# Kernel tuning notes

Measured on AMD Instinct MI355X. Metric: run time of the kernel, lower is better.

Reference implementation:

```python
import jax, jax.numpy as jnp
import numpy as np

N_NODES = 50000
N_EDGES = 1600000
IN_DIM, HIDDEN, OUT_DIM = 128, 128, 64


def setup_inputs() -> dict:
    key = jax.random.key(0)
    ks = jax.random.split(key, 8)
    x = jax.random.normal(ks[0], (N_NODES, IN_DIM), dtype=jnp.float32)
    edge_index = jax.random.randint(ks[1], (2, N_EDGES), 0, N_NODES, dtype=jnp.int64)
    # SAGEConv params: lin_l applied to aggregated neighbors (with bias),
    # lin_r applied to root/self features (no bias) -- PyG defaults.
    def lin_init(k, fan_in, fan_out):
        bound = 1.0 / np.sqrt(fan_in)
        return jax.random.uniform(k, (fan_in, fan_out), jnp.float32, -bound, bound)
    W1_l = lin_init(ks[2], IN_DIM, HIDDEN)
    W1_r = lin_init(ks[3], IN_DIM, HIDDEN)
    b1 = jnp.zeros((HIDDEN,), jnp.float32)
    W2_l = lin_init(ks[4], HIDDEN, OUT_DIM)
    W2_r = lin_init(ks[5], HIDDEN, OUT_DIM)
    b2 = jnp.zeros((OUT_DIM,), jnp.float32)
    return {"x": x, "edge_index": edge_index, "W1_l": W1_l, "W1_r": W1_r,
            "b1": b1, "W2_l": W2_l, "W2_r": W2_r, "b2": b2}


def _sage_conv(h, src, dst, n_nodes, W_l, W_r, b):
    # gather messages from source nodes, mean-aggregate at destinations
    msg = h[src]                                              # [E, D]
    agg_sum = jax.ops.segment_sum(msg, dst, num_segments=n_nodes)
    deg = jax.ops.segment_sum(jnp.ones((src.shape[0],), h.dtype), dst,
                              num_segments=n_nodes)
    agg_mean = agg_sum / jnp.maximum(deg, 1.0)[:, None]       # [N, D]
    return agg_mean @ W_l + h @ W_r + b


def reference(x, edge_index, W1_l, W1_r, b1, W2_l, W2_r, b2):
    n = x.shape[0]
    src, dst = edge_index[0], edge_index[1]
    h = jax.nn.relu(_sage_conv(x, src, dst, n, W1_l, W1_r, b1))
    return _sage_conv(h, src, dst, n, W2_l, W2_r, b2)
```

## Files before the change

### kernel.cpp

```cpp
#include <hip/hip_runtime.h>

#define NN 50000
#define NE 1600000
#define BSTRIDE 96
#define C_BKT 196
#define P1_BLKS 512
#define P1_CHUNK 3125
#define CAP 56
#define XCVT_BLKS 1563
#define WCVT_BLKS 48
#define PP_PREP (XCVT_BLKS + WCVT_BLKS)

typedef __bf16 bf16x8 __attribute__((ext_vector_type(8)));
typedef float  f32x4  __attribute__((ext_vector_type(4)));
typedef float  f32x2  __attribute__((ext_vector_type(2)));

__device__ __forceinline__ float bfLo(uint u) { union { uint i; float f; } v; v.i = u << 16; return v.f; }
__device__ __forceinline__ float bfHi(uint u) { union { uint i; float f; } v; v.i = u & 0xffff0000u; return v.f; }
__device__ __forceinline__ float bf1(ushort s) { union { uint i; float f; } v; v.i = (uint)s << 16; return v.f; }
__device__ __forceinline__ ushort f2bf(float f) {
    union { float f; uint i; } v; v.f = f;
    uint r = v.i + 0x7fffu + ((v.i >> 16) & 1u);
    return (ushort)(r >> 16);
}
__device__ __forceinline__ uint pack2(float a, float b) {
    return (uint)f2bf(a) | ((uint)f2bf(b) << 16);
}
__device__ __forceinline__ bf16x8 load8(const ushort* p) {
    union { uint4 u; bf16x8 b; } v; v.u = *(const uint4*)p; return v.b;
}

#define ACC8(u) { a0 += bfLo(u.x); a1 += bfHi(u.x); a2 += bfLo(u.y); a3 += bfHi(u.y); \
                  a4 += bfLo(u.z); a5 += bfHi(u.z); a6 += bfLo(u.w); a7 += bfHi(u.w); }

#define CVA(u, o) { f32x2 p0 = __builtin_amdgcn_cvt_pk_f32_fp8((int)(u), 0); \
                    f32x2 p1 = __builtin_amdgcn_cvt_pk_f32_fp8((int)(u), 1); \
                    a[(o)+0] += p0.x; a[(o)+1] += p0.y; a[(o)+2] += p1.x; a[(o)+3] += p1.y; }
#define ACCF8(v) { CVA((v).x, 0); CVA((v).y, 4); CVA((v).z, 8); CVA((v).w, 12); }

__global__ __launch_bounds__(1024) void k_pp(
    const float4* __restrict__ x, ushort4* __restrict__ xb, uint* __restrict__ xf8,
    const float* __restrict__ W1l, const float* __restrict__ W1r,
    const float* __restrict__ W2l, const float* __restrict__ W2r,
    ushort* __restrict__ T1l, ushort* __restrict__ T1r,
    ushort* __restrict__ T2l, ushort* __restrict__ T2r,
    const int* __restrict__ src, const int* __restrict__ dst,
    uint* __restrict__ cells, ushort* __restrict__ cnt) {
    __shared__ uint hist[C_BKT];
    const int b = blockIdx.x;
    const int tid = threadIdx.x;
    if (b < XCVT_BLKS) {
        int i = b * 1024 + tid;
        if (i < NN * 128 / 4) {
            float4 v = x[i];
            ushort4 o; o.x = f2bf(v.x); o.y = f2bf(v.y); o.z = f2bf(v.z); o.w = f2bf(v.w);
            xb[i] = o;
            uint r = (uint)__builtin_amdgcn_cvt_pk_fp8_f32(v.x, v.y, 0, 0);
            r = (uint)__builtin_amdgcn_cvt_pk_fp8_f32(v.z, v.w, (int)r, 1);
            xf8[i] = r;
        }
    } else if (b < PP_PREP) {
        int i = (b - XCVT_BLKS) * 1024 + tid;
        if (i < 16384) {
            int k = i >> 7, n = i & 127; T1l[n * 128 + k] = f2bf(W1l[i]);
        } else if (i < 32768) {
            int j = i - 16384; int k = j >> 7, n = j & 127; T1r[n * 128 + k] = f2bf(W1r[j]);
        } else if (i < 40960) {
            int j = i - 32768; int k = j >> 6, n = j & 63;  T2l[n * 128 + k] = f2bf(W2l[j]);
        } else {
            int j = i - 40960; int k = j >> 6, n = j & 63;  T2r[n * 128 + k] = f2bf(W2r[j]);
        }
    } else {
        const int b2 = b - PP_PREP;
        for (int i = tid; i < C_BKT; i += 1024) hist[i] = 0;
        __syncthreads();
        const int beg = b2 * P1_CHUNK;
        uint* myCells = cells + (size_t)b2 * C_BKT * CAP;
        for (int i = beg + tid; i < beg + P1_CHUNK; i += 1024) {
            int d = dst[i];
            int s = src[i];
            int c = d >> 8;
            uint p = atomicAdd(&hist[c], 1);
            if (p < CAP) myCells[c * CAP + p] = ((uint)(d & 255) << 16) | (uint)s;
        }
        __syncthreads();
        for (int i = tid; i < C_BKT; i += 1024)
            cnt[(size_t)b2 * C_BKT + i] = (ushort)min(hist[i], (uint)CAP);
    }
}

__global__ __launch_bounds__(1024) void k_part2(const uint* __restrict__ cells,
                        const ushort* __restrict__ cnt,
                        ushort* __restrict__ col, int* __restrict__ deg) {
    __shared__ uint hist[256];
    const int c = blockIdx.x;
    if (threadIdx.x < 256) hist[threadIdx.x] = 0;
    __syncthreads();
    const int b = threadIdx.x >> 1;
    const int sub = threadIdx.x & 1;
    const uint* cell = cells + ((size_t)b * C_BKT + c) * CAP;
    const int n = cnt[(size_t)b * C_BKT + c];
    const int nodeBase = c << 8;
    for (int j = sub; j < n; j += 2) {
        uint e = cell[j];
        int dl = e >> 16;
        uint p = atomicAdd(&hist[dl], 1);
        if (p < BSTRIDE)
            col[(size_t)(nodeBase + dl) * BSTRIDE + p] = (ushort)(e & 0xFFFF);
    }
    __syncthreads();
    if (threadIdx.x < 256) {
        int node = nodeBase + threadIdx.x;
        if (node < NN) deg[node] = (int)hist[threadIdx.x];
    }
}

__global__ void k_agg128(const uchar* __restrict__ xf8, const ushort* __restrict__ col,
                         const int* __restrict__ deg, ushort* __restrict__ out) {
    int node = (blockIdx.x * blockDim.x + threadIdx.x) >> 6;
    int lane = threadIdx.x & 63;
    int q = lane >> 3;
    int c = lane & 7;
    int d = deg[node];
    int dd = min(d, BSTRIDE);
    const ushort* cb = col + (size_t)node * BSTRIDE;
    float a[16];
    #pragma unroll
    for (int i = 0; i < 16; i++) a[i] = 0.f;
    for (int j0 = 0; j0 < dd; j0 += 64) {
        int idx = (j0 + lane < dd) ? (int)cb[j0 + lane] : 0;
        int cnt = min(64, dd - j0);
        int t = 0;
        for (; t + 16 <= cnt; t += 16) {
            int s0 = __shfl(idx, t + q);
            int s1 = __shfl(idx, t + 8 + q);
            uint4 u0 = *(const uint4*)(xf8 + (size_t)s0 * 128 + c * 16);
            uint4 u1 = *(const uint4*)(xf8 + (size_t)s1 * 128 + c * 16);
            ACCF8(u0); ACCF8(u1);
        }
        for (; t < cnt; t += 8) {
            int s = __shfl(idx, t + q);
            if (t + q < cnt) {
                uint4 u = *(const uint4*)(xf8 + (size_t)s * 128 + c * 16);
                ACCF8(u);
            }
        }
    }
    #pragma unroll
    for (int m = 8; m < 64; m <<= 1) {
        #pragma unroll
        for (int i = 0; i < 16; i++) a[i] += __shfl_xor(a[i], m);
    }
    if (q == 0) {
        float inv = 1.f / fmaxf((float)d, 1.f);
        uint4 o;
        o.x = pack2(a[0] * inv, a[1] * inv);
        o.y = pack2(a[2] * inv, a[3] * inv);
        o.z = pack2(a[4] * inv, a[5] * inv);
        o.w = pack2(a[6] * inv, a[7] * inv);
        *(uint4*)(out + (size_t)node * 128 + c * 16) = o;
        o.x = pack2(a[8] * inv, a[9] * inv);
        o.y = pack2(a[10] * inv, a[11] * inv);
        o.z = pack2(a[12] * inv, a[13] * inv);
        o.w = pack2(a[14] * inv, a[15] * inv);
        *(uint4*)(out + (size_t)node * 128 + c * 16 + 8) = o;
    }
}

#define PAD1 136
__global__ __launch_bounds__(256) void k_gemm12(
    const ushort* __restrict__ agg, const ushort* __restrict__ xb,
    const ushort* __restrict__ T1l, const ushort* __restrict__ T1r,
    const ushort* __restrict__ T2l, const ushort* __restrict__ T2r,
    const float* __restrict__ b1, const float* __restrict__ b2,
    ushort* __restrict__ hW, float* __restrict__ outp) {
    __shared__ ushort hS[2][16 * PAD1];
    const int lane = threadIdx.x & 63;
    const int wave = threadIdx.x >> 6;
    const int s = wave >> 1;
    const int ch = wave & 1;
    const int quad = lane >> 4, r16 = lane & 15;
    const int row0 = blockIdx.x * 32 + s * 16;
    const int arow = min(row0 + r16, NN - 1);
    ushort* myS = &hS[s][0];

    bf16x8 aAgg[4], aXb[4];
    #pragma unroll
    for (int kt = 0; kt < 4; kt++) {
        const int k = kt * 32 + quad * 8;
        aAgg[kt] = load8(agg + (size_t)arow * 128 + k);
        aXb[kt]  = load8(xb  + (size_t)arow * 128 + k);
    }

    f32x4 acc[4];
    #pragma unroll
    for (int nt = 0; nt < 4; nt++) acc[nt] = (f32x4){0.f, 0.f, 0.f, 0.f};
    #pragma unroll
    for (int kt = 0; kt < 4; kt++) {
        const int k = kt * 32 + quad * 8;
        #pragma unroll
        for (int nt = 0; nt < 4; nt++) {
            const int wr = ch * 64 + nt * 16 + r16;
            acc[nt] = __builtin_amdgcn_mfma_f32_16x16x32_bf16(aAgg[kt], load8(T1l + wr * 128 + k), acc[nt], 0, 0, 0);
            acc[nt] = __builtin_amdgcn_mfma_f32_16x16x32_bf16(aXb[kt],  load8(T1r + wr * 128 + k), acc[nt], 0, 0, 0);
        }
    }
    #pragma unroll
    for (int nt = 0; nt < 4; nt++) {
        int cc = ch * 64 + nt * 16 + r16;
        float bv = b1[cc];
        #pragma unroll
        for (int i = 0; i < 4; i++) {
            int lr = quad * 4 + i;
            myS[lr * PAD1 + cc] = f2bf(fmaxf(acc[nt][i] + bv, 0.f));
        }
    }
    __syncthreads();

    bf16x8 ah[4];
    #pragma unroll
    for (int kt = 0; kt < 4; kt++)
        ah[kt] = load8(&myS[r16 * PAD1 + kt * 32 + quad * 8]);

    f32x4 acc2[2], acc3[2];
    #pragma unroll
    for (int nt = 0; nt < 2; nt++) {
        acc2[nt] = (f32x4){0.f, 0.f, 0.f, 0.f};
        acc3[nt] = (f32x4){0.f, 0.f, 0.f, 0.f};
    }
    #pragma unroll
    for (int kt = 0; kt < 4; kt++) {
        const int k = kt * 32 + quad * 8;
        #pragma unroll
        for (int nt = 0; nt < 2; nt++) {
            const int wr = ch * 32 + nt * 16 + r16;
            acc2[nt] = __builtin_amdgcn_mfma_f32_16x16x32_bf16(ah[kt], load8(T2l + wr * 128 + k), acc2[nt], 0, 0, 0);
            acc3[nt] = __builtin_amdgcn_mfma_f32_16x16x32_bf16(ah[kt], load8(T2r + wr * 128 + k), acc3[nt], 0, 0, 0);
        }
    }
    #pragma unroll
    for (int nt = 0; nt < 2; nt++) {
        int cc = ch * 32 + nt * 16 + r16;
        float bv = b2[cc];
        #pragma unroll
        for (int i = 0; i < 4; i++) {
            int rr = row0 + quad * 4 + i;
            if (rr < NN) {
                hW[(size_t)rr * 64 + cc] = f2bf(acc2[nt][i]);
                outp[(size_t)rr * 64 + cc] = acc3[nt][i] + bv;
            }
        }
    }
}

__global__ void k_agg64f(const ushort* __restrict__ hW, const ushort* __restrict__ col,
                         const int* __restrict__ deg, const float* __restrict__ outp,
                         float* __restrict__ out) {
    int node = (blockIdx.x * blockDim.x + threadIdx.x) >> 6;
    int lane = threadIdx.x & 63;
    int q = lane >> 3;
    int c = lane & 7;
    int d = deg[node];
    int dd = min(d, BSTRIDE);
    const ushort* cb = col + (size_t)node * BSTRIDE;
    float a0=0.f,a1=0.f,a2=0.f,a3=0.f,a4=0.f,a5=0.f,a6=0.f,a7=0.f;
    for (int j0 = 0; j0 < dd; j0 += 64) {
        int idx = (j0 + lane < dd) ? (int)cb[j0 + lane] : 0;
        int cnt = min(64, dd - j0);
        int t = 0;
        for (; t + 16 <= cnt; t += 16) {
            int s0 = __shfl(idx, t + q);
            int s1 = __shfl(idx, t + 8 + q);
            uint4 u0 = *(const uint4*)(hW + (size_t)s0 * 64 + c * 8);
            uint4 u1 = *(const uint4*)(hW + (size_t)s1 * 64 + c * 8);
            ACC8(u0); ACC8(u1);
        }
        for (; t < cnt; t += 8) {
            int s = __shfl(idx, t + q);
            if (t + q < cnt) {
                uint4 u = *(const uint4*)(hW + (size_t)s * 64 + c * 8);
                ACC8(u);
            }
        }
    }
    #pragma unroll
    for (int m = 8; m < 64; m <<= 1) {
        a0 += __shfl_xor(a0, m); a1 += __shfl_xor(a1, m);
        a2 += __shfl_xor(a2, m); a3 += __shfl_xor(a3, m);
        a4 += __shfl_xor(a4, m); a5 += __shfl_xor(a5, m);
        a6 += __shfl_xor(a6, m); a7 += __shfl_xor(a7, m);
    }
    if (q == 0) {
        float inv = 1.f / fmaxf((float)d, 1.f);
        float4 p0 = *(const float4*)(outp + (size_t)node * 64 + c * 8);
        float4 p1 = *(const float4*)(outp + (size_t)node * 64 + c * 8 + 4);
        float4 o;
        o.x = a0 * inv + p0.x; o.y = a1 * inv + p0.y;
        o.z = a2 * inv + p0.z; o.w = a3 * inv + p0.w;
        *(float4*)(out + (size_t)node * 64 + c * 8) = o;
        o.x = a4 * inv + p1.x; o.y = a5 * inv + p1.y;
        o.z = a6 * inv + p1.z; o.w = a7 * inv + p1.w;
        *(float4*)(out + (size_t)node * 64 + c * 8 + 4) = o;
    }
}

extern "C" void kernel_launch(void* const* d_in, const int* in_sizes, int n_in,
                              void* d_out, int out_size, void* d_ws, size_t ws_size,
                              hipStream_t stream) {
    const float* x   = (const float*)d_in[0];
    const int*   ei  = (const int*)d_in[1];
    const float* W1l = (const float*)d_in[2];
    const float* W1r = (const float*)d_in[3];
    const float* b1  = (const float*)d_in[4];
    const float* W2l = (const float*)d_in[5];
    const float* W2r = (const float*)d_in[6];
    const float* b2  = (const float*)d_in[7];
    float* out = (float*)d_out;

    const int* src = ei;
    const int* dst = ei + NE;

    char* w = (char*)d_ws;
    ushort* col   = (ushort*)w;                  w += (size_t)NN * BSTRIDE * 2;
    int* deg      = (int*)w;                     w += (size_t)50048 * 4;
    ushort* cnt   = (ushort*)w;                  w += (size_t)P1_BLKS * C_BKT * 2;
    ushort* xb    = (ushort*)w;                  w += (size_t)NN * 128 * 2;
    ushort* T1l   = (ushort*)w;                  w += 128 * 128 * 2;
    ushort* T1r   = (ushort*)w;                  w += 128 * 128 * 2;
    ushort* T2l   = (ushort*)w;                  w += 64 * 128 * 2;
    ushort* T2r   = (ushort*)w;                  w += 64 * 128 * 2;
    ushort* agg1  = (ushort*)w;                  w += (size_t)NN * 128 * 2;
    ushort* hW    = (ushort*)w;                  w += (size_t)NN * 64 * 2;
    float* outp   = (float*)w;                   w += (size_t)NN * 64 * 4;
    uchar* xf8    = (uchar*)w;                   w += (size_t)NN * 128;
    uint* cells  = (uint*)agg1;

    k_pp<<<PP_PREP + P1_BLKS, 1024, 0, stream>>>(
        (const float4*)x, (ushort4*)xb, (uint*)xf8, W1l, W1r, W2l, W2r,
        T1l, T1r, T2l, T2r, src, dst, cells, cnt);
    k_part2<<<C_BKT, 1024, 0, stream>>>(cells, cnt, col, deg);

    k_agg128<<<NN / 4, 256, 0, stream>>>(xf8, col, deg, agg1);
    k_gemm12<<<(NN + 31) / 32, 256, 0, stream>>>(agg1, xb, T1l, T1r, T2l, T2r, b1, b2, hW, outp);

    k_agg64f<<<NN / 4, 256, 0, stream>>>(hW, col, deg, outp, out);
}
```

Before: 221.8 us.

## Store layer-2 messages as FP8 and root term as bf16, prefetch GEMM weights

The layer-2 projected features hW are now written as FP8 (e4m3) instead of bf16, and the root/bias partial outp as bf16 instead of fp32. This halves the gathered bytes in the second aggregation kernel, which now has each lane read 16 FP8 values and uses a 16-lane-per-edge layout. The GEMM kernel also preloads all weight fragments into registers before the MFMA loops and declares launch_bounds(256,1). This trades output accuracy for bandwidth, and higher register pressure may lower occupancy.

After: 236.1 us. 6.4% more time.

```diff
diff --git a/kernel.cpp b/kernel.cpp
--- a/kernel.cpp
+++ b/kernel.cpp
@@ -29,9 +29,9 @@
 __device__ __forceinline__ bf16x8 load8(const ushort* p) {
     union { uint4 u; bf16x8 b; } v; v.u = *(const uint4*)p; return v.b;
 }
-
-#define ACC8(u) { a0 += bfLo(u.x); a1 += bfHi(u.x); a2 += bfLo(u.y); a3 += bfHi(u.y); \
-                  a4 += bfLo(u.z); a5 += bfHi(u.z); a6 += bfLo(u.w); a7 += bfHi(u.w); }
+__device__ __forceinline__ uchar f2fp8(float v) {
+    return (uchar)((uint)__builtin_amdgcn_cvt_pk_fp8_f32(v, v, 0, 0) & 0xffu);
+}
 
 #define CVA(u, o) { f32x2 p0 = __builtin_amdgcn_cvt_pk_f32_fp8((int)(u), 0); \
                     f32x2 p1 = __builtin_amdgcn_cvt_pk_f32_fp8((int)(u), 1); \
@@ -168,12 +168,12 @@
 }
 
 #define PAD1 136
-__global__ __launch_bounds__(256) void k_gemm12(
+__global__ __launch_bounds__(256, 1) void k_gemm12(
     const ushort* __restrict__ agg, const ushort* __restrict__ xb,
     const ushort* __restrict__ T1l, const ushort* __restrict__ T1r,
     const ushort* __restrict__ T2l, const ushort* __restrict__ T2r,
     const float* __restrict__ b1, const float* __restrict__ b2,
-    ushort* __restrict__ hW, float* __restrict__ outp) {
+    uchar* __restrict__ hW8, ushort* __restrict__ outp) {
     __shared__ ushort hS[2][16 * PAD1];
     const int lane = threadIdx.x & 63;
     const int wave = threadIdx.x >> 6;
@@ -184,44 +184,51 @@
     const int arow = min(row0 + r16, NN - 1);
     ushort* myS = &hS[s][0];
 
-    bf16x8 aAgg[4], aXb[4];
+    bf16x8 aAgg[4], aXb[4], bl[4][4], br[4][4];
     #pragma unroll
     for (int kt = 0; kt < 4; kt++) {
         const int k = kt * 32 + quad * 8;
         aAgg[kt] = load8(agg + (size_t)arow * 128 + k);
         aXb[kt]  = load8(xb  + (size_t)arow * 128 + k);
-    }
-
-    f32x4 acc[4];
-    #pragma unroll
-    for (int nt = 0; nt < 4; nt++) acc[nt] = (f32x4){0.f, 0.f, 0.f, 0.f};
-    #pragma unroll
-    for (int kt = 0; kt < 4; kt++) {
-        const int k = kt * 32 + quad * 8;
         #pragma unroll
         for (int nt = 0; nt < 4; nt++) {
             const int wr = ch * 64 + nt * 16 + r16;
-            acc[nt] = __builtin_amdgcn_mfma_f32_16x16x32_bf16(aAgg[kt], load8(T1l + wr * 128 + k), acc[nt], 0, 0, 0);
-            acc[nt] = __builtin_amdgcn_mfma_f32_16x16x32_bf16(aXb[kt],  load8(T1r + wr * 128 + k), acc[nt], 0, 0, 0);
-        }
-    }
+            bl[kt][nt] = load8(T1l + wr * 128 + k);
+            br[kt][nt] = load8(T1r + wr * 128 + k);
+        }
+    }
+    f32x4 acc[4];
+    #pragma unroll
+    for (int nt = 0; nt < 4; nt++) acc[nt] = (f32x4){0.f, 0.f, 0.f, 0.f};
+    #pragma unroll
+    for (int kt = 0; kt < 4; kt++)
+        #pragma unroll
+        for (int nt = 0; nt < 4; nt++) {
+            acc[nt] = __builtin_amdgcn_mfma_f32_16x16x32_bf16(aAgg[kt], bl[kt][nt], acc[nt], 0, 0, 0);
+            acc[nt] = __builtin_amdgcn_mfma_f32_16x16x32_bf16(aXb[kt],  br[kt][nt], acc[nt], 0, 0, 0);
+        }
     #pragma unroll
     for (int nt = 0; nt < 4; nt++) {
         int cc = ch * 64 + nt * 16 + r16;
         float bv = b1[cc];
         #pragma unroll
-        for (int i = 0; i < 4; i++) {
-            int lr = quad * 4 + i;
-            myS[lr * PAD1 + cc] = f2bf(fmaxf(acc[nt][i] + bv, 0.f));
-        }
+        for (int i = 0; i < 4; i++)
+            myS[(quad * 4 + i) * PAD1 + cc] = f2bf(fmaxf(acc[nt][i] + bv, 0.f));
     }
     __syncthreads();
 
-    bf16x8 ah[4];
-    #pragma unroll
-    for (int kt = 0; kt < 4; kt++)
-        ah[kt] = load8(&myS[r16 * PAD1 + kt * 32 + quad * 8]);
-
+    bf16x8 ah[4], c2l[4][2], c2r[4][2];
+    #pragma unroll
+    for (int kt = 0; kt < 4; kt++) {
+        const int k = kt * 32 + quad * 8;
+        ah[kt] = load8(&myS[r16 * PAD1 + k]);
+        #pragma unroll
+        for (int nt = 0; nt < 2; nt++) {
+            const int wr = ch * 32 + nt * 16 + r16;
+            c2l[kt][nt] = load8(T2l + wr * 128 + k);
+            c2r[kt][nt] = load8(T2r + wr * 128 + k);
+        }
+    }
     f32x4 acc2[2], acc3[2];
     #pragma unroll
     for (int nt = 0; nt < 2; nt++) {
@@ -229,15 +236,12 @@
         acc3[nt] = (f32x4){0.f, 0.f, 0.f, 0.f};
     }
     #pragma unroll
-    for (int kt = 0; kt < 4; kt++) {
-        const int k = kt * 32 + quad * 8;
+    for (int kt = 0; kt < 4; kt++)
         #pragma unroll
         for (int nt = 0; nt < 2; nt++) {
-            const int wr = ch * 32 + nt * 16 + r16;
-            acc2[nt] = __builtin_amdgcn_mfma_f32_16x16x32_bf16(ah[kt], load8(T2l + wr * 128 + k), acc2[nt], 0, 0, 0);
-            acc3[nt] = __builtin_amdgcn_mfma_f32_16x16x32_bf16(ah[kt], load8(T2r + wr * 128 + k), acc3[nt], 0, 0, 0);
-        }
-    }
+            acc2[nt] = __builtin_amdgcn_mfma_f32_16x16x32_bf16(ah[kt], c2l[kt][nt], acc2[nt], 0, 0, 0);
+            acc3[nt] = __builtin_amdgcn_mfma_f32_16x16x32_bf16(ah[kt], c2r[kt][nt], acc3[nt], 0, 0, 0);
+        }
     #pragma unroll
     for (int nt = 0; nt < 2; nt++) {
         int cc = ch * 32 + nt * 16 + r16;
@@ -246,61 +250,67 @@
         for (int i = 0; i < 4; i++) {
             int rr = row0 + quad * 4 + i;
             if (rr < NN) {
-                hW[(size_t)rr * 64 + cc] = f2bf(acc2[nt][i]);
-                outp[(size_t)rr * 64 + cc] = acc3[nt][i] + bv;
+                hW8[(size_t)rr * 64 + cc] = f2fp8(acc2[nt][i]);
+                outp[(size_t)rr * 64 + cc] = f2bf(acc3[nt][i] + bv);
             }
         }
     }
 }
 
-__global__ void k_agg64f(const ushort* __restrict__ hW, const ushort* __restrict__ col,
-                         const int* __restrict__ deg, const float* __restrict__ outp,
+__global__ void k_agg64f(const uchar* __restrict__ hW8, const ushort* __restrict__ col,
+                         const int* __restrict__ deg, const ushort* __restrict__ outp,
                          float* __restrict__ out) {
     int node = (blockIdx.x * blockDim.x + threadIdx.x) >> 6;
     int lane = threadIdx.x & 63;
-    int q = lane >> 3;
-    int c = lane & 7;
+    int q = lane >> 2;
+    int c = lane & 3;
     int d = deg[node];
     int dd = min(d, BSTRIDE);
     const ushort* cb = col + (size_t)node * BSTRIDE;
-    float a0=0.f,a1=0.f,a2=0.f,a3=0.f,a4=0.f,a5=0.f,a6=0.f,a7=0.f;
+    float a[16];
+    #pragma unroll
+    for (int i = 0; i < 16; i++) a[i] = 0.f;
     for (int j0 = 0; j0 < dd; j0 += 64) {
         int idx = (j0 + lane < dd) ? (int)cb[j0 + lane] : 0;
         int cnt = min(64, dd - j0);
         int t = 0;
-        for (; t + 16 <= cnt; t += 16) {
+        for (; t + 32 <= cnt; t += 32) {
             int s0 = __shfl(idx, t + q);
-            int s1 = __shfl(idx, t + 8 + q);
-            uint4 u0 = *(const uint4*)(hW + (size_t)s0 * 64 + c * 8);
-            uint4 u1 = *(const uint4*)(hW + (size_t)s1 * 64 + c * 8);
-            ACC8(u0); ACC8(u1);
-        }
-        for (; t < cnt; t += 8) {
+            int s1 = __shfl(idx, t + 16 + q);
+            uint4 u0 = *(const uint4*)(hW8 + (size_t)s0 * 64 + c * 16);
+            uint4 u1 = *(const uint4*)(hW8 + (size_t)s1 * 64 + c * 16);
+            ACCF8(u0); ACCF8(u1);
+        }
+        for (; t < cnt; t += 16) {
             int s = __shfl(idx, t + q);
             if (t + q < cnt) {
-                uint4 u = *(const uint4*)(hW + (size_t)s * 64 + c * 8);
-                ACC8(u);
+                uint4 u = *(const uint4*)(hW8 + (size_t)s * 64 + c * 16);
+                ACCF8(u);
             }
         }
     }
     #pragma unroll
-    for (int m = 8; m < 64; m <<= 1) {
-        a0 += __shfl_xor(a0, m); a1 += __shfl_xor(a1, m);
-        a2 += __shfl_xor(a2, m); a3 += __shfl_xor(a3, m);
-        a4 += __shfl_xor(a4, m); a5 += __shfl_xor(a5, m);
-        a6 += __shfl_xor(a6, m); a7 += __shfl_xor(a7, m);
+    for (int m = 4; m < 64; m <<= 1) {
+        #pragma unroll
+        for (int i = 0; i < 16; i++) a[i] += __shfl_xor(a[i], m);
     }
     if (q == 0) {
         float inv = 1.f / fmaxf((float)d, 1.f);
-        float4 p0 = *(const float4*)(outp + (size_t)node * 64 + c * 8);
-        float4 p1 = *(const float4*)(outp + (size_t)node * 64 + c * 8 + 4);
+        uint4 p0 = *(const uint4*)(outp + (size_t)node * 64 + c * 16);
+        uint4 p1 = *(const uint4*)(outp + (size_t)node * 64 + c * 16 + 8);
         float4 o;
-        o.x = a0 * inv + p0.x; o.y = a1 * inv + p0.y;
-        o.z = a2 * inv + p0.z; o.w = a3 * inv + p0.w;
-        *(float4*)(out + (size_t)node * 64 + c * 8) = o;
-        o.x = a4 * inv + p1.x; o.y = a5 * inv + p1.y;
-        o.z = a6 * inv + p1.z; o.w = a7 * inv + p1.w;
-        *(float4*)(out + (size_t)node * 64 + c * 8 + 4) = o;
+        o.x = a[0] * inv + bfLo(p0.x); o.y = a[1] * inv + bfHi(p0.x);
+        o.z = a[2] * inv + bfLo(p0.y); o.w = a[3] * inv + bfHi(p0.y);
+        *(float4*)(out + (size_t)node * 64 + c * 16) = o;
+        o.x = a[4] * inv + bfLo(p0.z); o.y = a[5] * inv + bfHi(p0.z);
+        o.z = a[6] * inv + bfLo(p0.w); o.w = a[7] * inv + bfHi(p0.w);
+        *(float4*)(out + (size_t)node * 64 + c * 16 + 4) = o;
+        o.x = a[8] * inv + bfLo(p1.x); o.y = a[9] * inv + bfHi(p1.x);
+        o.z = a[10] * inv + bfLo(p1.y); o.w = a[11] * inv + bfHi(p1.y);
+        *(float4*)(out + (size_t)node * 64 + c * 16 + 8) = o;
+        o.x = a[12] * inv + bfLo(p1.z); o.y = a[13] * inv + bfHi(p1.z);
+        o.z = a[14] * inv + bfLo(p1.w); o.w = a[15] * inv + bfHi(p1.w);
+        *(float4*)(out + (size_t)node * 64 + c * 16 + 12) = o;
     }
 }
 
@@ -330,8 +340,9 @@
     ushort* T2l   = (ushort*)w;                  w += 64 * 128 * 2;
     ushort* T2r   = (ushort*)w;                  w += 64 * 128 * 2;
     ushort* agg1  = (ushort*)w;                  w += (size_t)NN * 128 * 2;
-    ushort* hW    = (ushort*)w;                  w += (size_t)NN * 64 * 2;
-    float* outp   = (float*)w;                   w += (size_t)NN * 64 * 4;
+    uchar* hW8    = (uchar*)w;                   w += (size_t)NN * 64;
+    ushort* outp  = (ushort*)w;                  w += (size_t)NN * 64 * 2;
+    w += 131072;
     uchar* xf8    = (uchar*)w;                   w += (size_t)NN * 128;
     uint* cells  = (uint*)agg1;
 
@@ -341,7 +352,7 @@
     k_part2<<<C_BKT, 1024, 0, stream>>>(cells, cnt, col, deg);
 
     k_agg128<<<NN / 4, 256, 0, stream>>>(xf8, col, deg, agg1);
-    k_gemm12<<<(NN + 31) / 32, 256, 0, stream>>>(agg1, xb, T1l, T1r, T2l, T2r, b1, b2, hW, outp);
-
-    k_agg64f<<<NN / 4, 256, 0, stream>>>(hW, col, deg, outp, out);
-}
+    k_gemm12<<<(NN + 31) / 32, 256, 0, stream>>>(agg1, xb, T1l, T1r, T2l, T2r, b1, b2, hW8, outp);
+
+    k_agg64f<<<NN / 4, 256, 0, stream>>>(hW8, col, deg, outp, out);
+}
```

## Store GEMM operands in MFMA-fragment-packed layout for contiguous per-lane loads

Applied to the files above, without the earlier changes.

The bf16 copy of x, the aggregated features and the transposed weights are now written in a tile-packed layout, where each 16-row by 32-k MFMA fragment is one contiguous 512-element block. Each lane then loads its 8 bf16 values at lane*8, so a wave reads 1 KB contiguously instead of strided row segments. The producer kernels (prep and agg128) take on the layout transform in their scattered writes, and the workspace grows slightly because rows are padded to a multiple of 16.

Result: faster. 198.0 us (-10.7%).

```diff
diff --git a/kernel.cpp b/kernel.cpp
--- a/kernel.cpp
+++ b/kernel.cpp
@@ -10,6 +10,7 @@
 #define XCVT_BLKS 1563
 #define WCVT_BLKS 48
 #define PP_PREP (XCVT_BLKS + WCVT_BLKS)
+#define RGRP 3128
 
 typedef __bf16 bf16x8 __attribute__((ext_vector_type(8)));
 typedef float  f32x4  __attribute__((ext_vector_type(4)));
@@ -17,7 +18,6 @@
 
 __device__ __forceinline__ float bfLo(uint u) { union { uint i; float f; } v; v.i = u << 16; return v.f; }
 __device__ __forceinline__ float bfHi(uint u) { union { uint i; float f; } v; v.i = u & 0xffff0000u; return v.f; }
-__device__ __forceinline__ float bf1(ushort s) { union { uint i; float f; } v; v.i = (uint)s << 16; return v.f; }
 __device__ __forceinline__ ushort f2bf(float f) {
     union { float f; uint i; } v; v.f = f;
     uint r = v.i + 0x7fffu + ((v.i >> 16) & 1u);
@@ -38,8 +38,12 @@
                     a[(o)+0] += p0.x; a[(o)+1] += p0.y; a[(o)+2] += p1.x; a[(o)+3] += p1.y; }
 #define ACCF8(v) { CVA((v).x, 0); CVA((v).y, 4); CVA((v).z, 8); CVA((v).w, 12); }
 
+__device__ __forceinline__ int pkOff(int n, int k) {
+    return (((n >> 4) * 4 + (k >> 5)) * 512) + (((k >> 3) & 3) * 128) + ((n & 15) * 8) + (k & 7);
+}
+
 __global__ __launch_bounds__(1024) void k_pp(
-    const float4* __restrict__ x, ushort4* __restrict__ xb, uint* __restrict__ xf8,
+    const float4* __restrict__ x, ushort* __restrict__ xbp, uint* __restrict__ xf8,
     const float* __restrict__ W1l, const float* __restrict__ W1r,
     const float* __restrict__ W2l, const float* __restrict__ W2r,
     ushort* __restrict__ T1l, ushort* __restrict__ T1r,
@@ -53,22 +57,23 @@
         int i = b * 1024 + tid;
         if (i < NN * 128 / 4) {
             float4 v = x[i];
+            int r = i >> 5, k0 = (i & 31) * 4;
             ushort4 o; o.x = f2bf(v.x); o.y = f2bf(v.y); o.z = f2bf(v.z); o.w = f2bf(v.w);
-            xb[i] = o;
-            uint r = (uint)__builtin_amdgcn_cvt_pk_fp8_f32(v.x, v.y, 0, 0);
-            r = (uint)__builtin_amdgcn_cvt_pk_fp8_f32(v.z, v.w, (int)r, 1);
-            xf8[i] = r;
+            *(ushort4*)(xbp + pkOff(r & 0xFFFF, k0) + ((r >> 4) * 4 + (k0 >> 5)) * 0) = o;
+            uint rr = (uint)__builtin_amdgcn_cvt_pk_fp8_f32(v.x, v.y, 0, 0);
+            rr = (uint)__builtin_amdgcn_cvt_pk_fp8_f32(v.z, v.w, (int)rr, 1);
+            xf8[i] = rr;
         }
     } else if (b < PP_PREP) {
         int i = (b - XCVT_BLKS) * 1024 + tid;
         if (i < 16384) {
-            int k = i >> 7, n = i & 127; T1l[n * 128 + k] = f2bf(W1l[i]);
+            int k = i >> 7, n = i & 127; T1l[pkOff(n, k)] = f2bf(W1l[i]);
         } else if (i < 32768) {
-            int j = i - 16384; int k = j >> 7, n = j & 127; T1r[n * 128 + k] = f2bf(W1r[j]);
+            int j = i - 16384; int k = j >> 7, n = j & 127; T1r[pkOff(n, k)] = f2bf(W1r[j]);
         } else if (i < 40960) {
-            int j = i - 32768; int k = j >> 6, n = j & 63;  T2l[n * 128 + k] = f2bf(W2l[j]);
+            int j = i - 32768; int k = j >> 6, n = j & 63;  T2l[pkOff(n, k)] = f2bf(W2l[j]);
         } else {
-            int j = i - 40960; int k = j >> 6, n = j & 63;  T2r[n * 128 + k] = f2bf(W2r[j]);
+            int j = i - 40960; int k = j >> 6, n = j & 63;  T2r[pkOff(n, k)] = f2bf(W2r[j]);
         }
     } else {
         const int b2 = b - PP_PREP;
@@ -116,7 +121,7 @@
 }
 
 __global__ void k_agg128(const uchar* __restrict__ xf8, const ushort* __restrict__ col,
-                         const int* __restrict__ deg, ushort* __restrict__ out) {
+                         const int* __restrict__ deg, ushort* __restrict__ aggp) {
     int node = (blockIdx.x * blockDim.x + threadIdx.x) >> 6;
     int lane = threadIdx.x & 63;
     int q = lane >> 3;
@@ -153,23 +158,24 @@
     }
     if (q == 0) {
         float inv = 1.f / fmaxf((float)d, 1.f);
+        int base = ((node >> 4) * 4 + (c >> 1)) * 512 + ((c & 1) * 2) * 128 + (node & 15) * 8;
         uint4 o;
         o.x = pack2(a[0] * inv, a[1] * inv);
         o.y = pack2(a[2] * inv, a[3] * inv);
         o.z = pack2(a[4] * inv, a[5] * inv);
         o.w = pack2(a[6] * inv, a[7] * inv);
-        *(uint4*)(out + (size_t)node * 128 + c * 16) = o;
+        *(uint4*)(aggp + base) = o;
         o.x = pack2(a[8] * inv, a[9] * inv);
         o.y = pack2(a[10] * inv, a[11] * inv);
         o.z = pack2(a[12] * inv, a[13] * inv);
         o.w = pack2(a[14] * inv, a[15] * inv);
-        *(uint4*)(out + (size_t)node * 128 + c * 16 + 8) = o;
+        *(uint4*)(aggp + base + 128) = o;
     }
 }
 
 #define PAD1 136
 __global__ __launch_bounds__(256) void k_gemm12(
-    const ushort* __restrict__ agg, const ushort* __restrict__ xb,
+    const ushort* __restrict__ aggp, const ushort* __restrict__ xbp,
     const ushort* __restrict__ T1l, const ushort* __restrict__ T1r,
     const ushort* __restrict__ T2l, const ushort* __restrict__ T2r,
     const float* __restrict__ b1, const float* __restrict__ b2,
@@ -181,28 +187,21 @@
     const int ch = wave & 1;
     const int quad = lane >> 4, r16 = lane & 15;
     const int row0 = blockIdx.x * 32 + s * 16;
-    const int arow = min(row0 + r16, NN - 1);
+    const int g = blockIdx.x * 2 + s;
     ushort* myS = &hS[s][0];
 
-    bf16x8 aAgg[4], aXb[4];
+    f32x4 acc[4];
+    #pragma unroll
+    for (int nt = 0; nt < 4; nt++) acc[nt] = (f32x4){0.f, 0.f, 0.f, 0.f};
     #pragma unroll
     for (int kt = 0; kt < 4; kt++) {
-        const int k = kt * 32 + quad * 8;
-        aAgg[kt] = load8(agg + (size_t)arow * 128 + k);
-        aXb[kt]  = load8(xb  + (size_t)arow * 128 + k);
-    }
-
-    f32x4 acc[4];
-    #pragma unroll
-    for (int nt = 0; nt < 4; nt++) acc[nt] = (f32x4){0.f, 0.f, 0.f, 0.f};
-    #pragma unroll
-    for (int kt = 0; kt < 4; kt++) {
-        const int k = kt * 32 + quad * 8;
+        bf16x8 aAgg = load8(aggp + (size_t)(g * 4 + kt) * 512 + lane * 8);
+        bf16x8 aXb  = load8(xbp  + (size_t)(g * 4 + kt) * 512 + lane * 8);
         #pragma unroll
         for (int nt = 0; nt < 4; nt++) {
-            const int wr = ch * 64 + nt * 16 + r16;
-            acc[nt] = __builtin_amdgcn_mfma_f32_16x16x32_bf16(aAgg[kt], load8(T1l + wr * 128 + k), acc[nt], 0, 0, 0);
-            acc[nt] = __builtin_amdgcn_mfma_f32_16x16x32_bf16(aXb[kt],  load8(T1r + wr * 128 + k), acc[nt], 0, 0, 0);
+            const int tile = ((ch * 4 + nt) * 4 + kt) * 512 + lane * 8;
+            acc[nt] = __builtin_amdgcn_mfma_f32_16x16x32_bf16(aAgg, load8(T1l + tile), acc[nt], 0, 0, 0);
+            acc[nt] = __builtin_amdgcn_mfma_f32_16x16x32_bf16(aXb,  load8(T1r + tile), acc[nt], 0, 0, 0);
         }
     }
     #pragma unroll
@@ -210,17 +209,10 @@
         int cc = ch * 64 + nt * 16 + r16;
         float bv = b1[cc];
         #pragma unroll
-        for (int i = 0; i < 4; i++) {
-            int lr = quad * 4 + i;
-            myS[lr * PAD1 + cc] = f2bf(fmaxf(acc[nt][i] + bv, 0.f));
-        }
+        for (int i = 0; i < 4; i++)
+            myS[(quad * 4 + i) * PAD1 + cc] = f2bf(fmaxf(acc[nt][i] + bv, 0.f));
     }
     __syncthreads();
-
-    bf16x8 ah[4];
-    #pragma unroll
-    for (int kt = 0; kt < 4; kt++)
-        ah[kt] = load8(&myS[r16 * PAD1 + kt * 32 + quad * 8]);
 
     f32x4 acc2[2], acc3[2];
     #pragma unroll
@@ -230,12 +222,12 @@
     }
     #pragma unroll
     for (int kt = 0; kt < 4; kt++) {
-        const int k = kt * 32 + quad * 8;
+        bf16x8 ah = load8(&myS[r16 * PAD1 + kt * 32 + quad * 8]);
         #pragma unroll
         for (int nt = 0; nt < 2; nt++) {
-            const int wr = ch * 32 + nt * 16 + r16;
-            acc2[nt] = __builtin_amdgcn_mfma_f32_16x16x32_bf16(ah[kt], load8(T2l + wr * 128 + k), acc2[nt], 0, 0, 0);
-            acc3[nt] = __builtin_amdgcn_mfma_f32_16x16x32_bf16(ah[kt], load8(T2r + wr * 128 + k), acc3[nt], 0, 0, 0);
+            const int tile = ((ch * 2 + nt) * 4 + kt) * 512 + lane * 8;
+            acc2[nt] = __builtin_amdgcn_mfma_f32_16x16x32_bf16(ah, load8(T2l + tile), acc2[nt], 0, 0, 0);
+            acc3[nt] = __builtin_amdgcn_mfma_f32_16x16x32_bf16(ah, load8(T2r + tile), acc3[nt], 0, 0, 0);
         }
     }
     #pragma unroll
@@ -324,24 +316,24 @@
     ushort* col   = (ushort*)w;                  w += (size_t)NN * BSTRIDE * 2;
     int* deg      = (int*)w;                     w += (size_t)50048 * 4;
     ushort* cnt   = (ushort*)w;                  w += (size_t)P1_BLKS * C_BKT * 2;
-    ushort* xb    = (ushort*)w;                  w += (size_t)NN * 128 * 2;
+    ushort* xbp   = (ushort*)w;                  w += (size_t)RGRP * 2048 * 2;
     ushort* T1l   = (ushort*)w;                  w += 128 * 128 * 2;
     ushort* T1r   = (ushort*)w;                  w += 128 * 128 * 2;
     ushort* T2l   = (ushort*)w;                  w += 64 * 128 * 2;
     ushort* T2r   = (ushort*)w;                  w += 64 * 128 * 2;
-    ushort* agg1  = (ushort*)w;                  w += (size_t)NN * 128 * 2;
+    ushort* aggp  = (ushort*)w;                  w += (size_t)RGRP * 2048 * 2;
     ushort* hW    = (ushort*)w;                  w += (size_t)NN * 64 * 2;
     float* outp   = (float*)w;                   w += (size_t)NN * 64 * 4;
     uchar* xf8    = (uchar*)w;                   w += (size_t)NN * 128;
-    uint* cells  = (uint*)agg1;
+    uint* cells  = (uint*)aggp;
 
     k_pp<<<PP_PREP + P1_BLKS, 1024, 0, stream>>>(
-        (const float4*)x, (ushort4*)xb, (uint*)xf8, W1l, W1r, W2l, W2r,
+        (const float4*)x, xbp, (uint*)xf8, W1l, W1r, W2l, W2r,
         T1l, T1r, T2l, T2r, src, dst, cells, cnt);
     k_part2<<<C_BKT, 1024, 0, stream>>>(cells, cnt, col, deg);
 
-    k_agg128<<<NN / 4, 256, 0, stream>>>(xf8, col, deg, agg1);
-    k_gemm12<<<(NN + 31) / 32, 256, 0, stream>>>(agg1, xb, T1l, T1r, T2l, T2r, b1, b2, hW, outp);
+    k_agg128<<<NN / 4, 256, 0, stream>>>(xf8, col, deg, aggp);
+    k_gemm12<<<(NN + 31) / 32, 256, 0, stream>>>(aggp, xbp, T1l, T1r, T2l, T2r, b1, b2, hW, outp);
 
     k_agg64f<<<NN / 4, 256, 0, stream>>>(hW, col, deg, outp, out);
 }
```
